# Kernel tuning notes

Hardware: AMD Instinct MI355X
Metric: run time of the kernel (lower is better)

Reference implementation:

```python
import jax, jax.numpy as jnp
import numpy as np


def _chamfer_single_directional(x, y):
    """Mean over batch of mean over points of min_j ||x_i - y_j||^2.

    x: [B, N, 3] (predicted), y: [B, M, 3] (target).
    Matches pytorch3d chamfer_distance(x, y, single_directional=True)
    with norm=2, point_reduction='mean', batch_reduction='mean'.
    """
    x2 = jnp.sum(x * x, axis=-1)                      # [B, N]
    y2 = jnp.sum(y * y, axis=-1)                      # [B, M]
    cross = jnp.einsum('bnd,bmd->bnm', x, y)          # [B, N, M]
    d2 = x2[:, :, None] + y2[:, None, :] - 2.0 * cross  # squared L2
    min_d2 = jnp.min(d2, axis=2)                      # [B, N] nearest in y
    return jnp.mean(jnp.mean(min_d2, axis=1))         # scalar


def setup_inputs() -> dict:
    key = jax.random.key(0)
    k1, k2 = jax.random.split(key)
    v = jax.random.normal(k1, (4, 8192, 3), dtype=jnp.float32)
    v_pred = jax.random.normal(k2, (4, 8192, 3), dtype=jnp.float32)
    return {"v": v, "v_pred": v_pred}


def reference(v, v_pred):
    # forward: chamfer_distance(v_pred, v, single_directional=True)
    return _chamfer_single_directional(v_pred, v)
```

## Files before the change

### kernel.cpp

```cpp
#include <hip/hip_runtime.h>

#define BB 4
#define NN 8192
#define MM 8192
#define BN (BB * NN)

#define BLK 256
#define P   8
#define NX  (BLK*P)
#define S   64
#define MC  (MM/S)

#define KEY_C 128.0f

typedef float v2f __attribute__((ext_vector_type(2)));

#if defined(__has_builtin) && __has_builtin(__builtin_elementwise_fma)
#define VFMA(a, b, c) __builtin_elementwise_fma((a), (b), (c))
#else
static __device__ inline v2f VFMA(v2f a, v2f b, v2f c) {
    v2f r; r.x = __builtin_fmaf(a.x, b.x, c.x); r.y = __builtin_fmaf(a.y, b.y, c.y);
    return r;
}
#endif

__global__ __launch_bounds__(BLK) void chamfer_min_atomic(
    const float* __restrict__ y,
    const float* __restrict__ x,
    int* __restrict__ gkey)
{
    __shared__ __attribute__((aligned(16))) float ZX[MC];
    __shared__ __attribute__((aligned(16))) float ZY[MC];
    __shared__ __attribute__((aligned(16))) float ZZ[MC];
    __shared__ __attribute__((aligned(16))) float ZW[MC];

    const int t  = threadIdx.x;
    const int ib = blockIdx.x;
    const int s  = blockIdx.y;
    const int b  = blockIdx.z;

    const float* yb = y + ((size_t)b * MM + (size_t)s * MC) * 3;
    if (t < MC) {
        float y0 = yb[3*t + 0];
        float y1 = yb[3*t + 1];
        float y2 = yb[3*t + 2];
        ZX[t] = 2.0f * y0;
        ZY[t] = 2.0f * y1;
        ZZ[t] = 2.0f * y2;
        ZW[t] = __builtin_fmaf(y2, y2, __builtin_fmaf(y1, y1, y0*y0));
    }
    __syncthreads();

    float nx0[P], nx1[P], nx2[P], xx[P], best[P];
    const float* xb = x + ((size_t)b * NN + (size_t)ib * NX) * 3;
#pragma unroll
    for (int p = 0; p < P; ++p) {
        int i = t + p * BLK;
        float a0 = xb[3*i + 0];
        float a1 = xb[3*i + 1];
        float a2 = xb[3*i + 2];
        nx0[p] = -a0; nx1[p] = -a1; nx2[p] = -a2;
        xx[p] = __builtin_fmaf(a2, a2, __builtin_fmaf(a1, a1, a0*a0));
        best[p] = 3.4e38f;
    }

#pragma unroll 2
    for (int jj = 0; jj < MC; jj += 4) {
        float4 ax = ((const float4*)ZX)[jj >> 2];
        float4 ay = ((const float4*)ZY)[jj >> 2];
        float4 az = ((const float4*)ZZ)[jj >> 2];
        float4 aw = ((const float4*)ZW)[jj >> 2];
        v2f zx01 = {ax.x, ax.y}, zx23 = {ax.z, ax.w};
        v2f zy01 = {ay.x, ay.y}, zy23 = {ay.z, ay.w};
        v2f zz01 = {az.x, az.y}, zz23 = {az.z, az.w};
        v2f zw01 = {aw.x, aw.y}, zw23 = {aw.z, aw.w};
#pragma unroll
        for (int p = 0; p < P; ++p) {
            v2f s0 = {nx0[p], nx0[p]};
            v2f s1 = {nx1[p], nx1[p]};
            v2f s2 = {nx2[p], nx2[p]};
            v2f t01 = VFMA(s0, zx01, zw01);
            t01 = VFMA(s1, zy01, t01);
            t01 = VFMA(s2, zz01, t01);
            v2f t23 = VFMA(s0, zx23, zw23);
            t23 = VFMA(s1, zy23, t23);
            t23 = VFMA(s2, zz23, t23);
            float m3 = fminf(fminf(t01.x, t01.y), t23.x);
            best[p] = fminf(fminf(m3, t23.y), best[p]);
        }
    }

    int* gk = gkey + (size_t)b * NN + (size_t)ib * NX;
#pragma unroll
    for (int p = 0; p < P; ++p) {
        float d2  = best[p] + xx[p];
        float key = KEY_C - d2;
        atomicMax(&gk[t + p * BLK], __float_as_int(key));
    }
}

__global__ __launch_bounds__(1024) void final_sum(
    const int* __restrict__ gkey,
    float* __restrict__ out)
{
    const int t = threadIdx.x;
    const int4* g4 = (const int4*)gkey;
    float acc = 0.0f;
#pragma unroll
    for (int i = t; i < BN / 4; i += 1024) {
        int4 k = g4[i];
        acc += (KEY_C - __int_as_float(k.x)) + (KEY_C - __int_as_float(k.y))
             + (KEY_C - __int_as_float(k.z)) + (KEY_C - __int_as_float(k.w));
    }
    for (int off = 32; off > 0; off >>= 1) {
        acc += __shfl_down(acc, off, 64);
    }
    __shared__ float wsum[16];
    const int lane = t & 63;
    const int w    = t >> 6;
    if (lane == 0) wsum[w] = acc;
    __syncthreads();
    if (t == 0) {
        float tot = 0.0f;
#pragma unroll
        for (int i = 0; i < 16; ++i) tot += wsum[i];
        out[0] = tot * (1.0f / (float)BN);
    }
}

extern "C" void kernel_launch(void* const* d_in, const int* in_sizes, int n_in,
                              void* d_out, int out_size, void* d_ws, size_t ws_size,
                              hipStream_t stream) {
    const float* v      = (const float*)d_in[0];
    const float* v_pred = (const float*)d_in[1];
    float* out = (float*)d_out;

    int* gkey = (int*)d_ws;

    dim3 grid1(NN / NX, S, BB);
    chamfer_min_atomic<<<grid1, BLK, 0, stream>>>(v, v_pred, gkey);

    final_sum<<<1, 1024, 0, stream>>>(gkey, out);
}
```

Baseline: 76.62 us.

## Read target points directly from global memory instead of staging in LDS

```diff
diff --git a/kernel.cpp b/kernel.cpp
--- a/kernel.cpp
+++ b/kernel.cpp
@@ -24,34 +24,18 @@
 }
 #endif
 
-__global__ __launch_bounds__(BLK) void chamfer_min_atomic(
+__global__ __launch_bounds__(BLK, 4) void chamfer_min_atomic(
     const float* __restrict__ y,
     const float* __restrict__ x,
     int* __restrict__ gkey)
 {
-    __shared__ __attribute__((aligned(16))) float ZX[MC];
-    __shared__ __attribute__((aligned(16))) float ZY[MC];
-    __shared__ __attribute__((aligned(16))) float ZZ[MC];
-    __shared__ __attribute__((aligned(16))) float ZW[MC];
-
     const int t  = threadIdx.x;
     const int ib = blockIdx.x;
     const int s  = blockIdx.y;
     const int b  = blockIdx.z;
 
-    const float* yb = y + ((size_t)b * MM + (size_t)s * MC) * 3;
-    if (t < MC) {
-        float y0 = yb[3*t + 0];
-        float y1 = yb[3*t + 1];
-        float y2 = yb[3*t + 2];
-        ZX[t] = 2.0f * y0;
-        ZY[t] = 2.0f * y1;
-        ZZ[t] = 2.0f * y2;
-        ZW[t] = __builtin_fmaf(y2, y2, __builtin_fmaf(y1, y1, y0*y0));
-    }
-    __syncthreads();
-
-    float nx0[P], nx1[P], nx2[P], xx[P], best[P];
+    float best[P], xx[P];
+    v2f nx0[P], nx1[P], nx2[P];
     const float* xb = x + ((size_t)b * NN + (size_t)ib * NX) * 3;
 #pragma unroll
     for (int p = 0; p < P; ++p) {
@@ -59,32 +43,36 @@
         float a0 = xb[3*i + 0];
         float a1 = xb[3*i + 1];
         float a2 = xb[3*i + 2];
-        nx0[p] = -a0; nx1[p] = -a1; nx2[p] = -a2;
+        nx0[p] = (v2f){-2.0f*a0, -2.0f*a0};
+        nx1[p] = (v2f){-2.0f*a1, -2.0f*a1};
+        nx2[p] = (v2f){-2.0f*a2, -2.0f*a2};
         xx[p] = __builtin_fmaf(a2, a2, __builtin_fmaf(a1, a1, a0*a0));
         best[p] = 3.4e38f;
     }
 
+    const float4* y4 = (const float4*)(y + ((size_t)b * MM + (size_t)s * MC) * 3);
+
 #pragma unroll 2
-    for (int jj = 0; jj < MC; jj += 4) {
-        float4 ax = ((const float4*)ZX)[jj >> 2];
-        float4 ay = ((const float4*)ZY)[jj >> 2];
-        float4 az = ((const float4*)ZZ)[jj >> 2];
-        float4 aw = ((const float4*)ZW)[jj >> 2];
-        v2f zx01 = {ax.x, ax.y}, zx23 = {ax.z, ax.w};
-        v2f zy01 = {ay.x, ay.y}, zy23 = {ay.z, ay.w};
-        v2f zz01 = {az.x, az.y}, zz23 = {az.z, az.w};
-        v2f zw01 = {aw.x, aw.y}, zw23 = {aw.z, aw.w};
+    for (int g = 0; g < MC / 4; ++g) {
+        float4 A = y4[3*g + 0];
+        float4 Bv = y4[3*g + 1];
+        float4 Cv = y4[3*g + 2];
+        v2f p0 = {A.x,  A.w };
+        v2f p1 = {A.y,  Bv.x};
+        v2f p2 = {A.z,  Bv.y};
+        v2f q0 = {Bv.z, Cv.y};
+        v2f q1 = {Bv.w, Cv.z};
+        v2f q2 = {Cv.x, Cv.w};
+        v2f yy01 = VFMA(p2, p2, VFMA(p1, p1, p0 * p0));
+        v2f yy23 = VFMA(q2, q2, VFMA(q1, q1, q0 * q0));
 #pragma unroll
         for (int p = 0; p < P; ++p) {
-            v2f s0 = {nx0[p], nx0[p]};
-            v2f s1 = {nx1[p], nx1[p]};
-            v2f s2 = {nx2[p], nx2[p]};
-            v2f t01 = VFMA(s0, zx01, zw01);
-            t01 = VFMA(s1, zy01, t01);
-            t01 = VFMA(s2, zz01, t01);
-            v2f t23 = VFMA(s0, zx23, zw23);
-            t23 = VFMA(s1, zy23, t23);
-            t23 = VFMA(s2, zz23, t23);
+            v2f t01 = VFMA(nx0[p], p0, yy01);
+            t01 = VFMA(nx1[p], p1, t01);
+            t01 = VFMA(nx2[p], p2, t01);
+            v2f t23 = VFMA(nx0[p], q0, yy23);
+            t23 = VFMA(nx1[p], q1, t23);
+            t23 = VFMA(nx2[p], q2, t23);
             float m3 = fminf(fminf(t01.x, t01.y), t23.x);
             best[p] = fminf(fminf(m3, t23.y), best[p]);
         }
```

After: 78.65 us. 1.03x slower.
